# Performance work log

Measured on AMD Instinct MI355X. Metric: run time of the kernel, lower is better.

The kernel has to match this reference:

```python
import jax, jax.numpy as jnp
import numpy as np

HEAD_SIZE = 64
TOKEN_EMB = 768
BLOCK_SIZE = 4096


def setup_inputs() -> dict:
    key = jax.random.key(0)
    ks = jax.random.split(key, 7)
    s = 1.0 / np.sqrt(TOKEN_EMB)  # torch Linear default init scale
    x = jax.random.normal(ks[0], (4, BLOCK_SIZE, TOKEN_EMB), dtype=jnp.float32)
    Wk = jax.random.uniform(ks[1], (TOKEN_EMB, HEAD_SIZE), minval=-s, maxval=s, dtype=jnp.float32)
    bk = jax.random.uniform(ks[2], (HEAD_SIZE,), minval=-s, maxval=s, dtype=jnp.float32)
    Wq = jax.random.uniform(ks[3], (TOKEN_EMB, HEAD_SIZE), minval=-s, maxval=s, dtype=jnp.float32)
    bq = jax.random.uniform(ks[4], (HEAD_SIZE,), minval=-s, maxval=s, dtype=jnp.float32)
    Wv = jax.random.uniform(ks[5], (TOKEN_EMB, HEAD_SIZE), minval=-s, maxval=s, dtype=jnp.float32)
    bv = jax.random.uniform(ks[6], (HEAD_SIZE,), minval=-s, maxval=s, dtype=jnp.float32)
    return {"x": x, "Wk": Wk, "bk": bk, "Wq": Wq, "bq": bq, "Wv": Wv, "bv": bv}


def reference(x, Wk, bk, Wq, bq, Wv, bv):
    B, T, C = x.shape
    k = x @ Wk + bk  # [B, T, H]
    q = x @ Wq + bq  # [B, T, H]
    v = x @ Wv + bv  # [B, T, H]
    # NOTE: original computes k @ q^T (not q @ k^T) and scales by C**-0.5 with
    # C = token embedding size (not head size). Reproduce faithfully.
    scale = jnp.asarray(C, x.dtype) ** -0.5
    wei = jnp.einsum('bth,bsh->bts', k, q) * scale  # [B, T, T]
    causal = jnp.tril(jnp.ones((T, T), dtype=bool))
    wei = jnp.where(causal, wei, -jnp.inf)
    wei = jax.nn.softmax(wei, axis=-1)
    return jnp.einsum('bts,bsh->bth', wei, v)  # [B, T, H]
```

## Files before the change

kernel.cpp:

```cpp
#include <hip/hip_runtime.h>
#include <hip/hip_bf16.h>

#define T_SEQ 4096
#define C_EMB 768
#define HEAD  64

typedef short  short4v __attribute__((ext_vector_type(4)));
typedef short  short8  __attribute__((ext_vector_type(8)));
typedef float  floatx4 __attribute__((ext_vector_type(4)));
typedef unsigned int uint2v __attribute__((ext_vector_type(2)));

static __device__ __forceinline__ short f2bf(float v) {
    __hip_bfloat16 h = __float2bfloat16(v);
    return *reinterpret_cast<short*>(&h);
}


__global__ void wt_transpose_kernel(const float* __restrict__ Wk,
                                    const float* __restrict__ Wq,
                                    const float* __restrict__ Wv,
                                    short* __restrict__ Wf) {
    const int total = 12 * 24 * 64 * 8;
    for (int idx = blockIdx.x * blockDim.x + threadIdx.x; idx < total;
         idx += gridDim.x * blockDim.x) {
        int e    = idx & 7;
        int lane = (idx >> 3) & 63;
        int t    = idx >> 9;
        int kc   = t % 24;
        int j    = t / 24;
        int g    = j >> 2;
        int n    = (j & 3) * 16 + (lane & 15);
        int k    = kc * 32 + ((lane >> 4) & 3) * 8 + e;
        const float* W = (g == 0) ? Wk : (g == 1) ? Wq : Wv;
        Wf[idx] = f2bf(W[k * HEAD + n]);
    }
}

__global__ __launch_bounds__(256) void qkv_mfma(
    const float* __restrict__ x, const short* __restrict__ Wf,
    const float* __restrict__ bkp, const float* __restrict__ bqp,
    const float* __restrict__ bvp,
    short* __restrict__ Kf, short* __restrict__ Qf, short* __restrict__ Vf) {
    const float scale2 = 0.052058773f;
    __shared__ __align__(16) short xs[32][200];

    const int tid  = threadIdx.x;
    const int w    = tid >> 6;
    const int lane = tid & 63;
    const int ln15 = lane & 15, quad = lane >> 4;
    const int rows0 = blockIdx.x * 32;
    const int rw = (w & 1) * 16;
    const int jb = (w >> 1) * 6;

    floatx4 acc[6];
#pragma unroll
    for (int jj = 0; jj < 6; ++jj) acc[jj] = (floatx4){0.f, 0.f, 0.f, 0.f};

    for (int ch = 0; ch < 4; ++ch) {
        floatx4 stg[6];
#pragma unroll
        for (int i = 0; i < 6; ++i) {
            int o   = i * 1024 + tid * 4;
            int r   = o / 192;
            int col = o - r * 192;
            stg[i] = *(const floatx4*)(x + (size_t)(rows0 + r) * C_EMB +
                                       ch * 192 + col);
        }
#pragma unroll
        for (int i = 0; i < 6; ++i) {
            int o   = i * 1024 + tid * 4;
            int r   = o / 192;
            int col = o - r * 192;
            unsigned p01, p23;
            asm("v_cvt_pk_bf16_f32 %0, %1, %2" : "=v"(p01) : "v"(stg[i][0]), "v"(stg[i][1]));
            asm("v_cvt_pk_bf16_f32 %0, %1, %2" : "=v"(p23) : "v"(stg[i][2]), "v"(stg[i][3]));
            *(uint2v*)&xs[r][col] = (uint2v){p01, p23};
        }
        __syncthreads();

#pragma unroll
        for (int kc2 = 0; kc2 < 6; ++kc2) {
            int kcg = ch * 6 + kc2;
            short8 a = *(const short8*)&xs[rw + ln15][kc2 * 32 + quad * 8];
            short8 wf[6];
#pragma unroll
            for (int jj = 0; jj < 6; ++jj)
                wf[jj] = *(const short8*)(Wf +
                    ((size_t)((jb + jj) * 24 + kcg) * 64 + lane) * 8);
#pragma unroll
            for (int jj = 0; jj < 6; ++jj)
                acc[jj] = __builtin_amdgcn_mfma_f32_16x16x32_bf16(a, wf[jj], acc[jj], 0, 0, 0);
        }
        __syncthreads();
    }

#pragma unroll
    for (int jj = 0; jj < 6; ++jj) {
        int j  = jb + jj;
        int g  = j >> 2;
        int nl = (j & 3) * 16 + ln15;
        float bias = (g == 0 ? bkp : g == 1 ? bqp : bvp)[nl];
        int kh = nl >> 5;
        int hq = (nl >> 3) & 3;
        int he = nl & 7;
#pragma unroll
        for (int r = 0; r < 4; ++r) {
            int grow = rows0 + rw + quad * 4 + r;
            float v = acc[jj][r] + bias;
            if (g == 0) {
                int t16 = grow >> 4, tr = grow & 15;
                Kf[((size_t)(t16 * 2 + kh)) * 512 + (tr | (hq << 4)) * 8 + he] =
                    f2bf(v * scale2);
            } else if (g == 1) {
                int t16 = grow >> 4, tr = grow & 15;
                Qf[((size_t)(t16 * 2 + kh)) * 512 + (tr | (hq << 4)) * 8 + he] =
                    f2bf(v);
            } else {
                int b = grow >> 12, s = grow & 4095;
                int fid = ((s >> 6) * 4 + (nl >> 4)) * 2 + ((s >> 5) & 1);
                int lc  = (((s >> 3) & 3) << 4) | (nl & 15);
                Vf[((size_t)b << 18) + (size_t)fid * 512 + lc * 8 + (s & 7)] =
                    f2bf(v);
            }
        }
    }
}

__global__ __launch_bounds__(64) void attn_part(
    const short* __restrict__ Kf, const short* __restrict__ Qf,
    const short* __restrict__ Vf, float* __restrict__ Oacc,
    float* __restrict__ lacc) {
    __shared__ __align__(16) short Ps[32][72];

    int lane = threadIdx.x & 63;
    int ln15 = lane & 15, quad = lane >> 4;
    int g32 = blockIdx.x, c = blockIdx.y, b = blockIdx.z;
    int dtile = g32 >> 1;
    int lo = c * 4;
    if (lo > dtile) return;
    int hi = min(dtile, lo + 3);
    int base = g32 * 32;

    short8 bk[2][2];
    {
        const short* kfp = Kf + ((size_t)(b * 256 + g32 * 2) * 2) * 512 + lane * 8;
#pragma unroll
        for (int tg = 0; tg < 2; ++tg)
#pragma unroll
            for (int kh = 0; kh < 2; ++kh)
                bk[tg][kh] = *(const short8*)(kfp + (tg * 2 + kh) * 512);
    }

    floatx4 o[2][4];
#pragma unroll
    for (int tg = 0; tg < 2; ++tg)
#pragma unroll
        for (int hb = 0; hb < 4; ++hb) o[tg][hb] = (floatx4){0.f, 0.f, 0.f, 0.f};
    float ls[2] = {0.f, 0.f};

    const short* qfp = Qf + ((size_t)(b * 256 + lo * 4) * 2) * 512 + lane * 8;
    const short* vfp = Vf + ((size_t)b << 18) + (size_t)lo * 8 * 512 + lane * 8;

    for (int st = lo; st <= hi; ++st) {
        short8 aq[4][2], bv[4][2];
#pragma unroll
        for (int sb = 0; sb < 4; ++sb)
#pragma unroll
            for (int kh = 0; kh < 2; ++kh)
                aq[sb][kh] = *(const short8*)(qfp + (sb * 2 + kh) * 512);
#pragma unroll
        for (int hb = 0; hb < 4; ++hb)
#pragma unroll
            for (int kh = 0; kh < 2; ++kh)
                bv[hb][kh] = *(const short8*)(vfp + (hb * 2 + kh) * 512);

        floatx4 sacc[4][2];
#pragma unroll
        for (int sb = 0; sb < 4; ++sb)
#pragma unroll
            for (int tg = 0; tg < 2; ++tg) {
                floatx4 z = (floatx4){0.f, 0.f, 0.f, 0.f};
                z = __builtin_amdgcn_mfma_f32_16x16x32_bf16(aq[sb][0], bk[tg][0], z, 0, 0, 0);
                z = __builtin_amdgcn_mfma_f32_16x16x32_bf16(aq[sb][1], bk[tg][1], z, 0, 0, 0);
                sacc[sb][tg] = z;
            }

        bool diag = (st == dtile);
        int s0 = st * 64;
#pragma unroll
        for (int tg = 0; tg < 2; ++tg) {
            int tgl = base + tg * 16 + ln15;
#pragma unroll
            for (int sb = 0; sb < 4; ++sb) {
                float pv[4];
#pragma unroll
                for (int r = 0; r < 4; ++r) {
                    float p = __builtin_amdgcn_exp2f(sacc[sb][tg][r]);
                    if (diag) {
                        int sg = s0 + sb * 16 + quad * 4 + r;
                        p = (sg > tgl) ? 0.f : p;
                    }
                    pv[r] = p;
                }
                ls[tg] += (pv[0] + pv[1]) + (pv[2] + pv[3]);
                unsigned a01, a23;
                asm("v_cvt_pk_bf16_f32 %0, %1, %2" : "=v"(a01) : "v"(pv[0]), "v"(pv[1]));
                asm("v_cvt_pk_bf16_f32 %0, %1, %2" : "=v"(a23) : "v"(pv[2]), "v"(pv[3]));
                *(uint2v*)&Ps[tg * 16 + ln15][sb * 16 + quad * 4] = (uint2v){a01, a23};
            }
        }
        __asm__ volatile("s_waitcnt lgkmcnt(0)" ::: "memory");
        short8 ap[2][2];
#pragma unroll
        for (int tg = 0; tg < 2; ++tg) {
            ap[tg][0] = *(const short8*)&Ps[tg * 16 + ln15][quad * 8];
            ap[tg][1] = *(const short8*)&Ps[tg * 16 + ln15][32 + quad * 8];
        }

#pragma unroll
        for (int tg = 0; tg < 2; ++tg)
#pragma unroll
            for (int hb = 0; hb < 4; ++hb) {
                o[tg][hb] = __builtin_amdgcn_mfma_f32_16x16x32_bf16(ap[tg][0], bv[hb][0], o[tg][hb], 0, 0, 0);
                o[tg][hb] = __builtin_amdgcn_mfma_f32_16x16x32_bf16(ap[tg][1], bv[hb][1], o[tg][hb], 0, 0, 0);
            }

        qfp += 8 * 512;
        vfp += 8 * 512;
    }

#pragma unroll
    for (int tg = 0; tg < 2; ++tg) {
        float v = ls[tg];
        v += __shfl_xor(v, 16, 64);
        v += __shfl_xor(v, 32, 64);
        if (quad == 0)
            atomicAdd(lacc + (size_t)b * T_SEQ + base + tg * 16 + ln15, v);
    }
#pragma unroll
    for (int tg = 0; tg < 2; ++tg)
#pragma unroll
        for (int r = 0; r < 4; ++r) {
            int t = base + tg * 16 + quad * 4 + r;
#pragma unroll
            for (int hb = 0; hb < 4; ++hb)
                atomicAdd(Oacc + ((size_t)(b * T_SEQ + t)) * HEAD + hb * 16 + ln15,
                          o[tg][hb][r]);
        }
}

__global__ __launch_bounds__(256) void attn_div(
    const float* __restrict__ Oacc, const float* __restrict__ lacc,
    float* __restrict__ out) {
    int idx = blockIdx.x * 256 + threadIdx.x;
    out[idx] = Oacc[idx] / lacc[idx >> 6];
}

extern "C" void kernel_launch(void* const* d_in, const int* in_sizes, int n_in,
                              void* d_out, int out_size, void* d_ws, size_t ws_size,
                              hipStream_t stream) {
    const int XSZ = 4 * T_SEQ * C_EMB;
    const int WSZ = C_EMB * HEAD;
    const int BSZ = HEAD;
    const float* x = nullptr;
    const float* W[3] = {nullptr, nullptr, nullptr};
    const float* B[3] = {nullptr, nullptr, nullptr};
    int iw = 0, ib = 0;
    for (int i = 0; i < n_in; ++i) {
        if (in_sizes[i] == XSZ) x = (const float*)d_in[i];
        else if (in_sizes[i] == WSZ && iw < 3) W[iw++] = (const float*)d_in[i];
        else if (in_sizes[i] == BSZ && ib < 3) B[ib++] = (const float*)d_in[i];
    }

    short* ws = (short*)d_ws;
    short* Kf = ws;
    short* Qf = Kf + (size_t)4 * T_SEQ * HEAD;
    short* Vf = Qf + (size_t)4 * T_SEQ * HEAD;
    short* Wf = Vf + (size_t)4 * HEAD * T_SEQ;
    float* Oacc = (float*)(Wf + (size_t)3 * HEAD * C_EMB);
    float* lacc = Oacc + (size_t)4 * T_SEQ * HEAD;

    hipMemsetAsync(Oacc, 0,
                   ((size_t)4 * T_SEQ * HEAD + 4 * T_SEQ) * sizeof(float),
                   stream);
    wt_transpose_kernel<<<96, 256, 0, stream>>>(W[0], W[1], W[2], Wf);
    qkv_mfma<<<512, 256, 0, stream>>>(x, Wf, B[0], B[1], B[2], Kf, Qf, Vf);
    attn_part<<<dim3(128, 16, 4), 64, 0, stream>>>(Kf, Qf, Vf, Oacc, lacc);
    attn_div<<<4096, 256, 0, stream>>>(Oacc, lacc, (float*)d_out);
}
```

Measured before the change: 155.7 us.

## Stage QKV outputs through LDS, double-buffer attention tiles, halve split count

The QKV projection epilogue now writes its bf16 results into shared memory in the fragment layout and then copies them to global memory as coalesced 16-byte stores, replacing scattered 2-byte stores. The attention kernel prefetches the next tile's Q and V fragments into a second register set while computing the current one. Each block now covers up to 8 key tiles instead of 4, and the grid's split dimension is halved to match, so fewer atomic partial-sum flushes are issued. The cost is higher register pressure and longer serial work per block, which may lower occupancy and parallelism.

```diff
diff --git a/kernel.cpp b/kernel.cpp
--- a/kernel.cpp
+++ b/kernel.cpp
@@ -94,33 +94,50 @@
         __syncthreads();
     }
 
+    short* lds = &xs[0][0];
 #pragma unroll
     for (int jj = 0; jj < 6; ++jj) {
         int j  = jb + jj;
         int g  = j >> 2;
         int nl = (j & 3) * 16 + ln15;
         float bias = (g == 0 ? bkp : g == 1 ? bqp : bvp)[nl];
-        int kh = nl >> 5;
-        int hq = (nl >> 3) & 3;
-        int he = nl & 7;
 #pragma unroll
         for (int r = 0; r < 4; ++r) {
-            int grow = rows0 + rw + quad * 4 + r;
+            int rloc = rw + quad * 4 + r;
             float v = acc[jj][r] + bias;
-            if (g == 0) {
-                int t16 = grow >> 4, tr = grow & 15;
-                Kf[((size_t)(t16 * 2 + kh)) * 512 + (tr | (hq << 4)) * 8 + he] =
-                    f2bf(v * scale2);
-            } else if (g == 1) {
-                int t16 = grow >> 4, tr = grow & 15;
-                Qf[((size_t)(t16 * 2 + kh)) * 512 + (tr | (hq << 4)) * 8 + he] =
-                    f2bf(v);
+            int off;
+            short val;
+            if (g == 2) {
+                val = f2bf(v);
+                off = 4096 + ((nl >> 4) << 9) +
+                      ((((rloc >> 3) & 3) << 4) | (nl & 15)) * 8 + (rloc & 7);
             } else {
-                int b = grow >> 12, s = grow & 4095;
-                int fid = ((s >> 6) * 4 + (nl >> 4)) * 2 + ((s >> 5) & 1);
-                int lc  = (((s >> 3) & 3) << 4) | (nl & 15);
-                Vf[((size_t)b << 18) + (size_t)fid * 512 + lc * 8 + (s & 7)] =
-                    f2bf(v);
+                val = (g == 0) ? f2bf(v * scale2) : f2bf(v);
+                int tr = rloc & 15, kh = nl >> 5;
+                int hq = (nl >> 3) & 3, he = nl & 7;
+                off = (g << 11) + (((rloc >> 4) * 2 + kh) << 9) +
+                      (tr | (hq << 4)) * 8 + he;
+            }
+            lds[off] = val;
+        }
+    }
+    __syncthreads();
+
+    {
+        int bb = rows0 >> 12, s = rows0 & 4095;
+        size_t vbase = ((size_t)bb << 18) +
+                       ((size_t)((s >> 6) * 8 + ((s >> 5) & 1)) << 9);
+#pragma unroll
+        for (int cc = 0; cc < 3; ++cc) {
+            int i = (cc * 256 + tid) * 8;
+            short8 d = *(const short8*)&lds[i];
+            if (i < 2048)
+                *(short8*)(Kf + (size_t)rows0 * 64 + i) = d;
+            else if (i < 4096)
+                *(short8*)(Qf + (size_t)rows0 * 64 + (i - 2048)) = d;
+            else {
+                int iv = i - 4096;
+                *(short8*)(Vf + vbase + (size_t)(iv >> 9) * 1024 + (iv & 511)) = d;
             }
         }
     }
@@ -136,9 +153,9 @@
     int ln15 = lane & 15, quad = lane >> 4;
     int g32 = blockIdx.x, c = blockIdx.y, b = blockIdx.z;
     int dtile = g32 >> 1;
-    int lo = c * 4;
+    int lo = c * 8;
     if (lo > dtile) return;
-    int hi = min(dtile, lo + 3);
+    int hi = min(dtile, lo + 7);
     int base = g32 * 32;
 
     short8 bk[2][2];
@@ -161,18 +178,35 @@
     const short* qfp = Qf + ((size_t)(b * 256 + lo * 4) * 2) * 512 + lane * 8;
     const short* vfp = Vf + ((size_t)b << 18) + (size_t)lo * 8 * 512 + lane * 8;
 
-    for (int st = lo; st <= hi; ++st) {
-        short8 aq[4][2], bv[4][2];
-#pragma unroll
-        for (int sb = 0; sb < 4; ++sb)
-#pragma unroll
-            for (int kh = 0; kh < 2; ++kh)
-                aq[sb][kh] = *(const short8*)(qfp + (sb * 2 + kh) * 512);
-#pragma unroll
-        for (int hb = 0; hb < 4; ++hb)
-#pragma unroll
-            for (int kh = 0; kh < 2; ++kh)
-                bv[hb][kh] = *(const short8*)(vfp + (hb * 2 + kh) * 512);
+    short8 aqA[4][2], bvA[4][2], aqB[4][2], bvB[4][2];
+#pragma unroll
+    for (int sb = 0; sb < 4; ++sb)
+#pragma unroll
+        for (int kh = 0; kh < 2; ++kh)
+            aqA[sb][kh] = *(const short8*)(qfp + (sb * 2 + kh) * 512);
+#pragma unroll
+    for (int hb = 0; hb < 4; ++hb)
+#pragma unroll
+        for (int kh = 0; kh < 2; ++kh)
+            bvA[hb][kh] = *(const short8*)(vfp + (hb * 2 + kh) * 512);
+
+    auto tile_step = [&](short8 (&aq)[4][2], short8 (&bv)[4][2],
+                         short8 (&aqn)[4][2], short8 (&bvn)[4][2], int st) {
+        if (st < hi) {
+            int ti = st + 1 - lo;
+#pragma unroll
+            for (int sb = 0; sb < 4; ++sb)
+#pragma unroll
+                for (int kh = 0; kh < 2; ++kh)
+                    aqn[sb][kh] = *(const short8*)(qfp + (size_t)ti * 4096 +
+                                                   (sb * 2 + kh) * 512);
+#pragma unroll
+            for (int hb = 0; hb < 4; ++hb)
+#pragma unroll
+                for (int kh = 0; kh < 2; ++kh)
+                    bvn[hb][kh] = *(const short8*)(vfp + (size_t)ti * 4096 +
+                                                   (hb * 2 + kh) * 512);
+        }
 
         floatx4 sacc[4][2];
 #pragma unroll
@@ -224,9 +258,14 @@
                 o[tg][hb] = __builtin_amdgcn_mfma_f32_16x16x32_bf16(ap[tg][0], bv[hb][0], o[tg][hb], 0, 0, 0);
                 o[tg][hb] = __builtin_amdgcn_mfma_f32_16x16x32_bf16(ap[tg][1], bv[hb][1], o[tg][hb], 0, 0, 0);
             }
-
-        qfp += 8 * 512;
-        vfp += 8 * 512;
+    };
+
+#pragma unroll
+    for (int it = 0; it < 8; it += 2) {
+        if (lo + it > hi) break;
+        tile_step(aqA, bvA, aqB, bvB, lo + it);
+        if (lo + it + 1 > hi) break;
+        tile_step(aqB, bvB, aqA, bvA, lo + it + 1);
     }
 
 #pragma unroll
@@ -285,6 +324,6 @@
                    stream);
     wt_transpose_kernel<<<96, 256, 0, stream>>>(W[0], W[1], W[2], Wf);
     qkv_mfma<<<512, 256, 0, stream>>>(x, Wf, B[0], B[1], B[2], Kf, Qf, Vf);
-    attn_part<<<dim3(128, 16, 4), 64, 0, stream>>>(Kf, Qf, Vf, Oacc, lacc);
+    attn_part<<<dim3(128, 8, 4), 64, 0, stream>>>(Kf, Qf, Vf, Oacc, lacc);
     attn_div<<<4096, 256, 0, stream>>>(Oacc, lacc, (float*)d_out);
 }
```

Result: no change. 155.0 us (-0.5%).
